# Kernel tuning notes

Measured on AMD Instinct MI355X. Metric: run time of the kernel, lower is better.

## Reference

```python
import jax
import jax.numpy as jnp
from jax import lax
import numpy as np

N_LAYER = 8
SCALE = 4
H_CH = 128
Z_CH = 64


def conv2d(x, w, b=None, stride=1, pad=0):
    # x: NCHW, w: OIHW
    out = lax.conv_general_dilated(
        x, w, (stride, stride), [(pad, pad), (pad, pad)],
        dimension_numbers=("NCHW", "OIHW", "NCHW"))
    if b is not None:
        out = out + b[None, :, None, None]
    return out


def conv_transpose2d(x, w, stride):
    # torch ConvTranspose2d semantics, weight shape (in, out, kH, kW), no bias
    return lax.conv_transpose(
        x, w, (stride, stride), "VALID",
        dimension_numbers=("NCHW", "IOHW", "NCHW"), transpose_kernel=True)


def lstm_cell(inp, hidden, cell, gw, gb, tw, tb):
    # inp = inp + transform(hidden); gates fused into one conv (order f,i,o,s)
    inp = inp + conv2d(hidden, tw, tb, pad=2)
    gates = conv2d(inp, gw, gb, pad=2)
    f, i, o, s = jnp.split(gates, 4, axis=1)
    cell = jax.nn.sigmoid(f) * cell + jax.nn.sigmoid(i) * jnp.tanh(s)
    hidden = jax.nn.sigmoid(o) * jnp.tanh(cell)
    return hidden, cell


def setup_inputs() -> dict:
    key = jax.random.key(0)
    ks = jax.random.split(key, 24)
    b, xc, H, W = 64, 3, 64, 64
    vd, rd = 7, 256
    hs, ws = H // SCALE, W // SCALE
    enc_in = vd + rd + xc + H_CH   # 394
    dec_in = vd + rd + Z_CH        # 327

    def w_init(k, shape):
        fan_in = int(np.prod(shape[1:]))
        return jax.random.normal(k, shape, jnp.float32) / np.sqrt(fan_in)

    inp = {
        "x": jax.random.normal(ks[0], (b, xc, H, W), jnp.float32),
        "v": jax.random.normal(ks[1], (b, vd), jnp.float32),
        "r": jax.random.normal(ks[2], (b, rd, hs, ws), jnp.float32),
        "eps": jax.random.normal(ks[3], (N_LAYER, b, Z_CH, hs, ws), jnp.float32),
        "read_w": w_init(ks[4], (xc, xc, SCALE, SCALE)),
        "write_w": w_init(ks[5], (H_CH, H_CH, SCALE, SCALE)),  # (in,out,kH,kW)
        "prior_w": w_init(ks[6], (2 * Z_CH, H_CH, 5, 5)),
        "prior_b": jnp.zeros((2 * Z_CH,), jnp.float32),
        "post_w": w_init(ks[7], (2 * Z_CH, H_CH, 5, 5)),
        "post_b": jnp.zeros((2 * Z_CH,), jnp.float32),
        "enc_gw": w_init(ks[8], (4 * H_CH, enc_in, 5, 5)),
        "enc_gb": jnp.zeros((4 * H_CH,), jnp.float32),
        "enc_tw": w_init(ks[9], (enc_in, H_CH, 5, 5)),
        "enc_tb": jnp.zeros((enc_in,), jnp.float32),
        "dec_gw": w_init(ks[10], (4 * H_CH, dec_in, 5, 5)),
        "dec_gb": jnp.zeros((4 * H_CH,), jnp.float32),
        "dec_tw": w_init(ks[11], (dec_in, H_CH, 5, 5)),
        "dec_tb": jnp.zeros((dec_in,), jnp.float32),
        "obs_w": w_init(ks[12], (xc, H_CH, 1, 1)),
        "obs_b": jnp.zeros((xc,), jnp.float32),
    }
    return inp


def reference(x, v, r, eps, read_w, write_w, prior_w, prior_b, post_w, post_b,
              enc_gw, enc_gb, enc_tw, enc_tb, dec_gw, dec_gb, dec_tw, dec_tb,
              obs_w, obs_b):
    b, _, H, W = x.shape
    hs, ws = H // SCALE, W // SCALE
    dt = x.dtype
    h_enc = jnp.zeros((b, H_CH, hs, ws), dt)
    c_enc = jnp.zeros((b, H_CH, hs, ws), dt)
    h_dec = jnp.zeros((b, H_CH, hs, ws), dt)
    c_dec = jnp.zeros((b, H_CH, hs, ws), dt)
    u = jnp.zeros((b, H_CH, H, W), dt)

    xr = conv2d(x, read_w, stride=SCALE)            # (b, xc, hs, ws)
    vb = jnp.broadcast_to(v[:, :, None, None], (b, v.shape[1], hs, ws))
    rb = r if r.shape[2] == hs else jnp.tile(r, (1, 1, hs, ws))

    kl_loss = jnp.zeros((), dt)
    for t in range(N_LAYER):
        p_mu, p_lv = jnp.split(conv2d(h_dec, prior_w, prior_b, pad=2), 2, axis=1)
        h_enc, c_enc = lstm_cell(
            jnp.concatenate([h_dec, xr, vb, rb], axis=1),
            h_enc, c_enc, enc_gw, enc_gb, enc_tw, enc_tb)
        q_mu, q_lv = jnp.split(conv2d(h_enc, post_w, post_b, pad=2), 2, axis=1)
        z = q_mu + jnp.exp(0.5 * q_lv) * eps[t]
        h_dec, c_dec = lstm_cell(
            jnp.concatenate([z, vb, rb], axis=1),
            h_dec, c_dec, dec_gw, dec_gb, dec_tw, dec_tb)
        u = u + conv_transpose2d(h_dec, write_w, SCALE)
        # KL(q||p) with var = exp(logvar); log(var1/var0) = p_lv - q_lv
        kl = 0.5 * (jnp.exp(q_lv - p_lv)
                    + (p_mu - q_mu) ** 2 * jnp.exp(-p_lv)
                    - 1.0 + (p_lv - q_lv))
        kl_loss = kl_loss + kl.sum(axis=(1, 2, 3)).mean()

    canvas = jax.nn.sigmoid(conv2d(u, obs_w, obs_b))
    return canvas, kl_loss
```

## Files before the change

### kernel.cpp

```cpp
#include <hip/hip_runtime.h>
#include <hip/hip_bf16.h>

using bf16 = __hip_bfloat16;
typedef __attribute__((ext_vector_type(8))) short short8;
typedef __attribute__((ext_vector_type(4))) float f32x4;
typedef __attribute__((ext_vector_type(8))) int i32x8;
typedef __attribute__((ext_vector_type(4))) int i32x4;

#define DEVI __device__ __forceinline__

#define MTOT 16384
#define PADS 25600

DEVI float sigm_(float x){ return 1.f/(1.f+expf(-x)); }

DEVI long pidx_(int m){
  int nb = m>>8, iy=(m>>4)&15, ix=m&15;
  return (long)(nb*20 + iy + 2)*20 + (ix + 2);
}

DEVI unsigned char f2fp8(float x){
  int p = __builtin_amdgcn_cvt_pk_fp8_f32(x, 0.f, 0, false);
  return (unsigned char)(p & 0xFF);
}
DEVI float fp82f(unsigned char v){
  return __builtin_amdgcn_cvt_f32_fp8((int)v, 0);
}

DEVI void async16(const void* g, void* l) {
  __builtin_amdgcn_global_load_lds(
      (__attribute__((address_space(1))) void*)(unsigned long long)g,
      (__attribute__((address_space(3))) void*)(unsigned int)(unsigned long long)l,
      16, 0, 0);
}

template<int N> DEVI void waitbar(){
  if constexpr (N==0)      asm volatile("s_waitcnt vmcnt(0)\ns_barrier" ::: "memory");
  else if constexpr (N==3) asm volatile("s_waitcnt vmcnt(3)\ns_barrier" ::: "memory");
  else                     asm volatile("s_waitcnt vmcnt(6)\ns_barrier" ::: "memory");
}

template<int CA, int NS>
DEVI void g8_core(const unsigned char* __restrict__ A8,
                  const unsigned char* __restrict__ Bt8,
                  int m0, int n0, unsigned char* AsB, unsigned char* BsB,
                  f32x4 (&acc)[4][4])
{
  constexpr int Kp8 = NS*128;
  const int tid = threadIdx.x;
  const int wv = tid>>6, ln = tid&63;

  const int rr = tid>>3;
  const int lc = (tid&7) ^ (rr&7);
  long paRC[4], pbR[4];
  #pragma unroll
  for (int i=0;i<4;i++){
    int m = m0 + rr + (i<<5);
    paRC[i] = (long)(((m>>8)*20 + ((m>>4)&15))*20 + (m&15)) * CA;
    pbR[i]  = (long)(n0 + rr + (i<<5))*Kp8 + lc*16;
  }

  int cc = lc*16, tp = 0, ks = 0;
  auto stage = [&](int d){
    const int shiftC = ((tp/5)*20 + (tp%5)) * CA;
    char* la = (char*)AsB + d*16384 + (wv<<10);
    char* lb = (char*)BsB + d*16384 + (wv<<10);
    #pragma unroll
    for (int i=0;i<4;i++) async16(A8 + paRC[i] + shiftC + cc, la + i*4096);
    #pragma unroll
    for (int i=0;i<4;i++) async16(Bt8 + pbR[i] + ks, lb + i*4096);
    cc += 128; if (cc >= CA){ cc -= CA; tp++; }
    ks += 128;
  };

  const int wm = wv>>1, wn = wv&1;
  const int rA0 = (wm<<6) + (ln&15);
  const int rB0 = (wn<<6) + (ln&15);
  const int xa = ln&7;
  const int q2 = (ln>>4)<<1;
  const int c0 = ((q2    ) ^ xa)<<4;
  const int c1 = ((q2 | 1) ^ xa)<<4;

  stage(0);
  for (int t=0; t<NS; ++t) {
    asm volatile("s_waitcnt vmcnt(0)\ns_barrier" ::: "memory");
    if (t+1 < NS) stage((t+1)&1);

    const char* as_ = (const char*)AsB + (t&1)*16384;
    const char* bs_ = (const char*)BsB + (t&1)*16384;
    i32x8 af[4], bfr[4];
    #pragma unroll
    for (int f=0; f<4; f++){
      const char* p = as_ + ((rA0 + (f<<4))<<7);
      ((i32x4*)&af[f])[0] = *(const i32x4*)(p + c0);
      ((i32x4*)&af[f])[1] = *(const i32x4*)(p + c1);
    }
    #pragma unroll
    for (int f=0; f<4; f++){
      const char* p = bs_ + ((rB0 + (f<<4))<<7);
      ((i32x4*)&bfr[f])[0] = *(const i32x4*)(p + c0);
      ((i32x4*)&bfr[f])[1] = *(const i32x4*)(p + c1);
    }
    __builtin_amdgcn_s_setprio(1);
    #pragma unroll
    for (int mf=0; mf<4; mf++)
      #pragma unroll
      for (int nf=0; nf<4; nf++)
        acc[mf][nf] = __builtin_amdgcn_mfma_scale_f32_16x16x128_f8f6f4(
            af[mf], bfr[nf], acc[mf][nf], 0, 0, 0, 127, 0, 122);
    __builtin_amdgcn_s_setprio(0);
  }
}

template<int CA, int NS>
__global__ __launch_bounds__(256)
void conv_g8(const unsigned char* __restrict__ A8,
             const unsigned char* __restrict__ Bt8,
             const float* __restrict__ bias, bf16* __restrict__ outB)
{
  __shared__ alignas(16) unsigned char As[2][16384];
  __shared__ alignas(16) unsigned char Bs[2][16384];
  const int m0 = blockIdx.x<<7, n0 = blockIdx.y<<7;
  f32x4 acc[4][4] = {};
  g8_core<CA,NS>(A8, Bt8, m0, n0, &As[0][0], &Bs[0][0], acc);

  const int tid = threadIdx.x;
  const int wv = tid>>6, ln = tid&63;
  const int mb = m0 + ((wv>>1)<<6);
  const int nb = n0 + ((wv&1)<<6);
  const int ml = (ln>>4)<<2;
  const int nl = ln&15;
  #pragma unroll
  for (int mf=0; mf<4; mf++)
    #pragma unroll
    for (int j=0; j<4; j++) {
      const int m = mb + (mf<<4) + ml + j;
      #pragma unroll
      for (int nf=0; nf<4; nf++) {
        const int n = nb + (nf<<4) + nl;
        outB[((long)m<<9) + n] = __float2bfloat16(acc[mf][nf][j] + bias[n]);
      }
    }
}

__global__ __launch_bounds__(256)
void conv_tp8(const unsigned char* __restrict__ h8Dec,
              const unsigned char* __restrict__ h8Enc,
              const unsigned char* __restrict__ Bt8DP,
              const unsigned char* __restrict__ Bt8EncT,
              const float* __restrict__ dec_tb, const float* __restrict__ prior_b,
              const float* __restrict__ enc_tb,
              float* __restrict__ PriorO,
              unsigned char* __restrict__ sDec8, const bf16* __restrict__ STdec,
              unsigned char* __restrict__ sEnc8, const bf16* __restrict__ STenc,
              const bf16* __restrict__ hDecB,
              const float* __restrict__ Wc, float* __restrict__ uc)
{
  __shared__ alignas(16) unsigned char As[2][16384];
  __shared__ alignas(16) unsigned char Bs[2][16384];
  const int z = blockIdx.z;
  const int m0 = blockIdx.x<<7, n0 = blockIdx.y<<7;
  f32x4 acc[4][4] = {};
  if (z == 0) g8_core<128,25>(h8Dec, Bt8DP,   m0, n0, &As[0][0], &Bs[0][0], acc);
  else        g8_core<128,25>(h8Enc, Bt8EncT, m0, n0, &As[0][0], &Bs[0][0], acc);

  const int tid = threadIdx.x;
  const int wv = tid>>6, ln = tid&63;
  const int mb = m0 + ((wv>>1)<<6);
  const int nb = n0 + ((wv&1)<<6);
  const int ml = (ln>>4)<<2;
  const int nl = ln&15;
  #pragma unroll
  for (int mf=0; mf<4; mf++)
    #pragma unroll
    for (int j=0; j<4; j++) {
      const int m = mb + (mf<<4) + ml + j;
      const long pI = pidx_(m);
      #pragma unroll
      for (int nf=0; nf<4; nf++) {
        const int n = nb + (nf<<4) + nl;
        const float v = acc[mf][nf][j];
        if (z == 0) {
          if (n < 352) {
            float b  = (n < 327) ? dec_tb[n] : 0.f;
            float st = __bfloat162float(STdec[(long)m*352 + n]);
            sDec8[pI*352 + n] = f2fp8(v + b + st);
          } else if (n >= 384) {
            PriorO[((long)m<<7) + (n-384)] = v + prior_b[n-384];
          }
        } else {
          if (n < 416) {
            float b  = (n < 394) ? enc_tb[n] : 0.f;
            float st = __bfloat162float(STenc[(long)m*416 + n]);
            float e  = (n < 128) ? __bfloat162float(hDecB[(pI<<7) + n]) : 0.f;
            sEnc8[pI*416 + n] = f2fp8(v + b + st + e);
          }
        }
      }
    }

  const int gid = blockIdx.z*512 + blockIdx.y*128 + blockIdx.x;
  const int m = (gid<<4) + (tid>>4);
  const int pix = tid&15;
  const int nb2 = m>>8, iy=(m>>4)&15, ix=m&15;
  const bf16* __restrict__ h = hDecB + (pidx_(m)<<7);
  float a0=0.f, a1=0.f, a2=0.f;
  #pragma unroll 4
  for (int c=0;c<128;c++) {
    float hv = __bfloat162float(h[c]);
    const float* wl = Wc + c*48 + pix*3;
    a0 += hv*wl[0]; a1 += hv*wl[1]; a2 += hv*wl[2];
  }
  const int ki = pix>>2, kj = pix&3;
  long ob = ((long)((nb2<<6) + (iy<<2) + ki)*64 + (ix<<2) + kj)*3;
  uc[ob+0] += a0; uc[ob+1] += a1; uc[ob+2] += a2;
}

template<int CA, int EPI>
DEVI void conv_body(const bf16* __restrict__ A, const bf16* __restrict__ Bt,
                    bf16* __restrict__ outB,
                    int s0, int s1, int m0, int n0,
                    bf16* AsBase, bf16* BsBase)
{
  constexpr int Kp = 25*CA;
  const int NS = s1 - s0;

  const int tid = threadIdx.x;
  const int wv = tid>>6, ln = tid&63;

  const int rA = tid>>2;
  const int qs = ((tid&3) ^ ((rA>>1)&3))<<3;
  const int mA0 = m0 + rA, mA1 = m0 + 128 + rA;
  const long paA0 = ((long)(((mA0>>8)*20 + ((mA0>>4)&15))*20 + (mA0&15)))*CA + qs;
  const long paA1 = ((long)(((mA1>>8)*20 + ((mA1>>4)&15))*20 + (mA1&15)))*CA + qs;
  const long pbB  = (long)(n0 + rA)*Kp + qs;

  int kk0 = s0*32;
  int c0 = kk0 % CA;
  int tap = kk0 / CA;
  int kh = tap/5, kw = tap%5;
  int ks = kk0;

  auto stage = [&](int d){
    const long sh = (long)(kh*20 + kw)*CA + c0;
    char* la = (char*)AsBase + d*16384 + (wv<<10);
    char* lb = (char*)BsBase + d*8192  + (wv<<10);
    async16(A + paA0 + sh, la);
    async16(A + paA1 + sh, la + 8192);
    async16(Bt + pbB + ks, lb);
    ks += 32;
    c0 += 32; if (c0==CA){ c0=0; if(++kw==5){kw=0; ++kh;} }
  };

  f32x4 acc[4][4] = {};
  const int wm = wv>>1, wn = wv&1;
  const int rowA = (wm<<6) + (ln&15);
  const int rowB = (wn<<6) + (ln&15);
  const int kqA = (((ln>>4) ^ ((rowA>>1)&3))<<4);
  const int kqB = (((ln>>4) ^ ((rowB>>1)&3))<<4);

  stage(0); stage(1);
  int bc = 0, bs = 2;
  for (int t=0; t<NS; ++t) {
    if (t+1 < NS) waitbar<3>();
    else          waitbar<0>();
    if (t+2 < NS) stage(bs);

    const char* as_ = (const char*)AsBase + bc*16384;
    const char* bs_ = (const char*)BsBase + bc*8192;
    short8 af[4], bfr[4];
    #pragma unroll
    for (int mf=0; mf<4; mf++)
      af[mf] = *(const short8*)(as_ + ((rowA + (mf<<4))<<6) + kqA);
    #pragma unroll
    for (int nf=0; nf<4; nf++)
      bfr[nf] = *(const short8*)(bs_ + ((rowB + (nf<<4))<<6) + kqB);
    __builtin_amdgcn_s_setprio(1);
    #pragma unroll
    for (int mf=0; mf<4; mf++)
      #pragma unroll
      for (int nf=0; nf<4; nf++)
        acc[mf][nf] = __builtin_amdgcn_mfma_f32_16x16x32_bf16(af[mf], bfr[nf], acc[mf][nf], 0,0,0);
    __builtin_amdgcn_s_setprio(0);
    bc = (bc==2)?0:bc+1; bs = (bs==2)?0:bs+1;
  }

  const int mb = m0 + (wm<<6);
  const int nb = n0 + (wn<<6);
  const int ml = (ln>>4)<<2;
  const int nl = ln&15;
  #pragma unroll
  for (int mf=0; mf<4; mf++)
    #pragma unroll
    for (int j=0; j<4; j++) {
      const int m = mb + (mf<<4) + ml + j;
      #pragma unroll
      for (int nf=0; nf<4; nf++) {
        const int n = nb + (nf<<4) + nl;
        outB[((long)m<<7) + n] = __float2bfloat16(acc[mf][nf][j]);
      }
    }
}

__global__ __launch_bounds__(512)
void conv_post(const bf16* __restrict__ hEnc, const bf16* __restrict__ BtPost,
               bf16* __restrict__ PP)
{
  __shared__ alignas(16) bf16 As[3][256*32];
  __shared__ alignas(16) bf16 Bs[3][128*32];
  const int z = blockIdx.z;
  conv_body<128,6>(hEnc, BtPost, PP + (long)z*MTOT*128,
                   z*25, z*25+25, blockIdx.x<<8, 0, &As[0][0], &Bs[0][0]);
}

__global__ void repack_w_k(const float* __restrict__ w, bf16* __restrict__ Bt,
                           int O, int I, int CA, long total)
{
  long e = (long)blockIdx.x*256 + threadIdx.x;
  if (e >= total) return;
  const int Kp = 25*CA;
  int o = (int)(e / Kp);
  int k = (int)(e % Kp);
  int blk = k / CA, c = k % CA;
  float v = 0.f;
  if (o < O && c < I) v = w[((long)o*I + c)*25 + blk];
  Bt[e] = __float2bfloat16(v);
}

__global__ void repack_w8_k(const float* __restrict__ w, unsigned char* __restrict__ Bt,
                            int O, int I, int CA, int Kp8, long total)
{
  long e = (long)blockIdx.x*256 + threadIdx.x;
  if (e >= total) return;
  int o = (int)(e / Kp8);
  int k = (int)(e % Kp8);
  float v = 0.f;
  if (k < 25*CA) {
    int blk = k / CA, c = k % CA;
    if (o < O && c < I) v = w[((long)o*I + c)*25 + blk] * 32.0f;
  }
  Bt[e] = f2fp8(v);
}

__global__ void wcomb_k(const float* __restrict__ ww, const float* __restrict__ ow,
                        float* __restrict__ Wc)
{
  int idx = blockIdx.x*256 + threadIdx.x;
  if (idx >= 128*48) return;
  int c = idx / 48, rst = idx % 48;
  int pix = rst / 3, o = rst % 3;
  int ki = pix >> 2, kj = pix & 3;
  float a = 0.f;
  for (int mm=0; mm<128; mm++)
    a += ww[(((long)c*128 + mm)*4 + ki)*4 + kj] * ow[o*128 + mm];
  Wc[idx] = a;
}

__global__ void xr_k(const float* __restrict__ x, const float* __restrict__ rw,
                     float* __restrict__ xr)
{
  int idx = blockIdx.x*256 + threadIdx.x;
  if (idx >= MTOT*3) return;
  int m = idx / 3, o = idx % 3;
  int nb = m>>8, iy=(m>>4)&15, ix=m&15;
  float a = 0.f;
  for (int c=0;c<3;c++)
    for (int kh=0;kh<4;kh++)
      for (int kw=0;kw<4;kw++)
        a += x[((long)(nb*3+c)*64 + (iy*4+kh))*64 + (ix*4+kw)] * rw[((o*3+c)*4+kh)*4+kw];
  xr[idx] = a;
}

__global__ void st_enc_k(const float* __restrict__ xr, const float* __restrict__ v,
                         const float* __restrict__ r, bf16* __restrict__ ST)
{
  long g = (long)blockIdx.x*256 + threadIdx.x;
  if (g >= (long)MTOT*266) return;
  int m = (int)(g / 266), ch = (int)(g % 266);
  int nb = m>>8, sp = m&255;
  float val;
  if (ch < 3)       val = xr[m*3 + ch];
  else if (ch < 10) val = v[nb*7 + ch - 3];
  else              val = r[((long)nb*256 + (ch-10))*256 + sp];
  ST[(long)m*416 + 128 + ch] = __float2bfloat16(val);
}

__global__ void st_dec_k(const float* __restrict__ v, const float* __restrict__ r,
                         bf16* __restrict__ ST)
{
  long g = (long)blockIdx.x*256 + threadIdx.x;
  if (g >= (long)MTOT*263) return;
  int m = (int)(g / 263), ch = (int)(g % 263);
  int nb = m>>8, sp = m&255;
  float val;
  if (ch < 7) val = v[nb*7 + ch];
  else        val = r[((long)nb*256 + (ch-7))*256 + sp];
  ST[(long)m*352 + 64 + ch] = __float2bfloat16(val);
}

__global__ void lstm_k(const bf16* __restrict__ gates, float* __restrict__ cbuf,
                       bf16* __restrict__ hpad, unsigned char* __restrict__ h8)
{
  int idx = blockIdx.x*256 + threadIdx.x;
  int m = idx >> 7, c = idx & 127;
  long gb = (long)m << 9;
  float f = __bfloat162float(gates[gb + c]);
  float i = __bfloat162float(gates[gb + 128 + c]);
  float o = __bfloat162float(gates[gb + 256 + c]);
  float s = __bfloat162float(gates[gb + 384 + c]);
  float cell = sigm_(f)*cbuf[idx] + sigm_(i)*tanhf(s);
  cbuf[idx] = cell;
  float h = sigm_(o)*tanhf(cell);
  long hp = (pidx_(m)<<7) + c;
  hpad[hp] = __float2bfloat16(h);
  h8[hp] = f2fp8(h);
}

__global__ void zkl4_k(const bf16* __restrict__ PP, const float* __restrict__ pb,
                       const float* __restrict__ prior, const float* __restrict__ eps_t,
                       unsigned char* __restrict__ sDec8, float* __restrict__ part)
{
  __shared__ float wsum[4];
  const long PL = (long)MTOT*128;
  int idx = blockIdx.x*256 + threadIdx.x;
  int m = idx >> 6, c = idx & 63;
  float qm = pb[c], ql = pb[64 + c];
  #pragma unroll
  for (int z=0; z<4; ++z) {
    qm += __bfloat162float(PP[z*PL + ((long)m<<7) + c]);
    ql += __bfloat162float(PP[z*PL + ((long)m<<7) + 64 + c]);
  }
  long pbx = (long)m << 7;
  float pm = prior[pbx + c], pl = prior[pbx + 64 + c];
  int nb = m>>8, sp = m&255;
  float e = eps_t[((long)nb*64 + c)*256 + sp];
  float z = qm + expf(0.5f*ql)*e;
  long so = pidx_(m)*352 + c;
  sDec8[so] = f2fp8(fp82f(sDec8[so]) + z);
  float kl = expf(ql - pl) + (pm-qm)*(pm-qm)*expf(-pl) - 1.f + (pl - ql);
  #pragma unroll
  for (int off=32; off>0; off>>=1) kl += __shfl_down(kl, off);
  if ((threadIdx.x & 63) == 0) wsum[threadIdx.x >> 6] = kl;
  __syncthreads();
  if (threadIdx.x == 0)
    part[blockIdx.x] = wsum[0] + wsum[1] + wsum[2] + wsum[3];
}

__global__ __launch_bounds__(256)
void wrc_k(const bf16* __restrict__ hpad, const float* __restrict__ Wc,
           float* __restrict__ uc)
{
  __shared__ float Wl[128*48];
  for (int i = threadIdx.x; i < 128*48; i += 256) Wl[i] = Wc[i];
  __syncthreads();
  int t = threadIdx.x;
  int mloc = t >> 4, pix = t & 15;
  int m = (blockIdx.x<<4) + mloc;
  int nb = m>>8, iy=(m>>4)&15, ix=m&15;
  const bf16* h = hpad + (pidx_(m)<<7);
  float a0=0.f, a1=0.f, a2=0.f;
  for (int c=0;c<128;c++) {
    float hv = __bfloat162float(h[c]);
    const float* wl = Wl + c*48 + pix*3;
    a0 += hv*wl[0]; a1 += hv*wl[1]; a2 += hv*wl[2];
  }
  int ki = pix>>2, kj = pix&3;
  long ob = ((long)((nb<<6) + (iy<<2) + ki)*64 + (ix<<2) + kj)*3;
  uc[ob+0] += a0; uc[ob+1] += a1; uc[ob+2] += a2;
}

__global__ void canvas_k(const float* __restrict__ uc, const float* __restrict__ ob,
                         float* __restrict__ out)
{
  int idx = blockIdx.x*256 + threadIdx.x;
  int x = idx & 63, y = (idx>>6)&63;
  int rem = idx >> 12;
  int o = rem % 3, n = rem / 3;
  float v = uc[((long)((n<<6)+y)*64 + x)*3 + o] + ob[o];
  out[idx] = 1.f/(1.f+expf(-v));
}

__global__ void klred_k(const float* __restrict__ part, float* __restrict__ out)
{
  __shared__ float wsum[4];
  float a = 0.f;
  for (int i = threadIdx.x; i < 32768; i += 256) a += part[i];
  #pragma unroll
  for (int off=32; off>0; off>>=1) a += __shfl_down(a, off);
  if ((threadIdx.x & 63) == 0) wsum[threadIdx.x >> 6] = a;
  __syncthreads();
  if (threadIdx.x == 0)
    out[786432] = (wsum[0] + wsum[1] + wsum[2] + wsum[3]) * (0.5f/64.f);
}

static const long O_BT_POST  = 0;
static const long O_BT_ENCT  = O_BT_POST  + 819200;
static const long O_BT_DP    = O_BT_ENCT  + 3276800;
static const long O_BT_ENCG  = O_BT_DP    + 3276800;
static const long O_BT_DECG  = O_BT_ENCG  + 10649600;
static const long O_WCOMB    = O_BT_DECG  + 9011200;
static const long O_XR       = O_WCOMB    + 24576;
static const long O_KLP      = O_XR       + 196608;
static const long O_STENC    = O_KLP      + 131072;
static const long O_STDEC    = O_STENC    + 13631488;
static const long O_HENC     = O_STDEC    + 11534336;
static const long O_HDEC     = O_HENC     + 6553600;
static const long O_SENC     = O_HDEC     + 6553600;
static const long O_SDEC     = O_SENC     + 21299200;
static const long O_CENC     = O_SDEC     + 18022400;
static const long O_CDEC     = O_CENC     + 8388608;
static const long O_PRIOR    = O_CDEC     + 8388608;
static const long O_H8E      = O_PRIOR    + 8388608;
static const long O_H8D      = O_H8E      + 3276800;
static const long O_PG       = O_H8D      + 3276800;
static const long O_UC       = O_PG       + 33554432;
static const long WS_TOTAL   = O_UC       + 3145728;

extern "C" void kernel_launch(void* const* d_in, const int* in_sizes, int n_in,
                              void* d_out, int out_size, void* d_ws, size_t ws_size,
                              hipStream_t stream)
{
  const float* x       = (const float*)d_in[0];
  const float* v       = (const float*)d_in[1];
  const float* r       = (const float*)d_in[2];
  const float* eps     = (const float*)d_in[3];
  const float* read_w  = (const float*)d_in[4];
  const float* write_w = (const float*)d_in[5];
  const float* prior_w = (const float*)d_in[6];
  const float* prior_b = (const float*)d_in[7];
  const float* post_w  = (const float*)d_in[8];
  const float* post_b  = (const float*)d_in[9];
  const float* enc_gw  = (const float*)d_in[10];
  const float* enc_gb  = (const float*)d_in[11];
  const float* enc_tw  = (const float*)d_in[12];
  const float* enc_tb  = (const float*)d_in[13];
  const float* dec_gw  = (const float*)d_in[14];
  const float* dec_gb  = (const float*)d_in[15];
  const float* dec_tw  = (const float*)d_in[16];
  const float* dec_tb  = (const float*)d_in[17];
  const float* obs_w   = (const float*)d_in[18];
  const float* obs_b   = (const float*)d_in[19];

  char* ws = (char*)d_ws;
  bf16* BtPost  = (bf16*)(ws + O_BT_POST);
  unsigned char* Bt8EncT = (unsigned char*)(ws + O_BT_ENCT);
  unsigned char* Bt8DP   = (unsigned char*)(ws + O_BT_DP);
  unsigned char* Bt8EncG = (unsigned char*)(ws + O_BT_ENCG);
  unsigned char* Bt8DecG = (unsigned char*)(ws + O_BT_DECG);
  float* Wcomb  = (float*)(ws + O_WCOMB);
  float* XR     = (float*)(ws + O_XR);
  float* KLpart = (float*)(ws + O_KLP);
  bf16* STenc   = (bf16*)(ws + O_STENC);
  bf16* STdec   = (bf16*)(ws + O_STDEC);
  bf16* hEnc    = (bf16*)(ws + O_HENC);
  bf16* hDec    = (bf16*)(ws + O_HDEC);
  unsigned char* sEnc8 = (unsigned char*)(ws + O_SENC);
  unsigned char* sDec8 = (unsigned char*)(ws + O_SDEC);
  float* cEnc   = (float*)(ws + O_CENC);
  float* cDec   = (float*)(ws + O_CDEC);
  float* PriorO = (float*)(ws + O_PRIOR);
  unsigned char* h8Enc = (unsigned char*)(ws + O_H8E);
  unsigned char* h8Dec = (unsigned char*)(ws + O_H8D);
  bf16* Gates   = (bf16*)(ws + O_PG);
  bf16* PostP   = (bf16*)(ws + O_PG + 16777216);
  float* Ucomb  = (float*)(ws + O_UC);
  float* out    = (float*)d_out;

  size_t clr = (size_t)WS_TOTAL; if (clr > ws_size) clr = ws_size;
  hipMemsetAsync(d_ws, 0, clr, stream);

  repack_w_k<<<1600, 256, 0, stream>>>(post_w, BtPost, 128, 128, 128, 128L*3200);
  repack_w8_k<<<6400, 256, 0, stream>>>(enc_tw, Bt8EncT, 394, 128, 128, 3200, 512L*3200);
  repack_w8_k<<<4800, 256, 0, stream>>>(dec_tw, Bt8DP, 327, 128, 128, 3200, 384L*3200);
  repack_w8_k<<<1600, 256, 0, stream>>>(prior_w, Bt8DP + 384L*3200, 128, 128, 128, 3200, 128L*3200);
  repack_w8_k<<<20992, 256, 0, stream>>>(enc_gw, Bt8EncG, 512, 394, 416, 82*128, 512L*10496);
  repack_w8_k<<<17664, 256, 0, stream>>>(dec_gw, Bt8DecG, 512, 327, 352, 69*128, 512L*8832);
  wcomb_k<<<24, 256, 0, stream>>>(write_w, obs_w, Wcomb);
  xr_k<<<192, 256, 0, stream>>>(x, read_w, XR);
  st_enc_k<<<(int)(((long)MTOT*266 + 255)/256), 256, 0, stream>>>(XR, v, r, STenc);
  st_dec_k<<<(int)(((long)MTOT*263 + 255)/256), 256, 0, stream>>>(v, r, STdec);

  for (int t = 0; t < 8; ++t) {
    conv_tp8<<<dim3(128,4,2), 256, 0, stream>>>(
        h8Dec, h8Enc, Bt8DP, Bt8EncT, dec_tb, prior_b, enc_tb,
        PriorO, sDec8, STdec, sEnc8, STenc, hDec, Wcomb, Ucomb);
    conv_g8<416,82><<<dim3(128,4), 256, 0, stream>>>(sEnc8, Bt8EncG, enc_gb, Gates);
    lstm_k<<<8192, 256, 0, stream>>>(Gates, cEnc, hEnc, h8Enc);
    conv_post<<<dim3(64,1,4), 512, 0, stream>>>(hEnc, BtPost, PostP);
    zkl4_k<<<4096, 256, 0, stream>>>(PostP, post_b, PriorO,
                                     eps + (long)t*64*64*256, sDec8,
                                     KLpart + (long)t*4096);
    conv_g8<352,69><<<dim3(128,4), 256, 0, stream>>>(sDec8, Bt8DecG, dec_gb, Gates);
    lstm_k<<<8192, 256, 0, stream>>>(Gates, cDec, hDec, h8Dec);
  }

  wrc_k<<<1024, 256, 0, stream>>>(hDec, Wcomb, Ucomb);
  canvas_k<<<3072, 256, 0, stream>>>(Ucomb, obs_b, out);
  klred_k<<<1, 256, 0, stream>>>(KLpart, out);
}
```

Baseline: 2.685 ms.

## Vectorize LSTM kernel and fuse write-conv accumulation into decoder LSTM

The LSTM pointwise kernel now handles 8 channels per thread, using 16-byte gate loads, vector cell-state loads and stores, and packed fp8 writes. The per-step canvas write convolution, which used to sit at the tail of conv_tp8 and read hDec from global memory, moves into a new lstm_wrc_k kernel. That kernel stages the fresh decoder hidden state and the combined weights in shared memory and accumulates into Ucomb right after the decoder LSTM. This removes the extra work from the GEMM kernel's epilogue and the separate final wrc_k launch. In exchange, each LSTM block now loads the 24KB weight table into LDS on every step.

New measurement: 2.620 ms. 2.5% less time.

```diff
diff --git a/kernel.cpp b/kernel.cpp
--- a/kernel.cpp
+++ b/kernel.cpp
@@ -6,6 +6,7 @@
 typedef __attribute__((ext_vector_type(4))) float f32x4;
 typedef __attribute__((ext_vector_type(8))) int i32x8;
 typedef __attribute__((ext_vector_type(4))) int i32x4;
+typedef __attribute__((ext_vector_type(2))) int i32x2;
 
 #define DEVI __device__ __forceinline__
 
@@ -13,6 +14,11 @@
 #define PADS 25600
 
 DEVI float sigm_(float x){ return 1.f/(1.f+expf(-x)); }
+
+DEVI float s2f(short v){
+  unsigned u = ((unsigned)(unsigned short)v) << 16;
+  return __builtin_bit_cast(float, u);
+}
 
 DEVI long pidx_(int m){
   int nb = m>>8, iy=(m>>4)&15, ix=m&15;
@@ -153,8 +159,7 @@
               float* __restrict__ PriorO,
               unsigned char* __restrict__ sDec8, const bf16* __restrict__ STdec,
               unsigned char* __restrict__ sEnc8, const bf16* __restrict__ STenc,
-              const bf16* __restrict__ hDecB,
-              const float* __restrict__ Wc, float* __restrict__ uc)
+              const bf16* __restrict__ hDecB)
 {
   __shared__ alignas(16) unsigned char As[2][16384];
   __shared__ alignas(16) unsigned char Bs[2][16384];
@@ -198,22 +203,6 @@
         }
       }
     }
-
-  const int gid = blockIdx.z*512 + blockIdx.y*128 + blockIdx.x;
-  const int m = (gid<<4) + (tid>>4);
-  const int pix = tid&15;
-  const int nb2 = m>>8, iy=(m>>4)&15, ix=m&15;
-  const bf16* __restrict__ h = hDecB + (pidx_(m)<<7);
-  float a0=0.f, a1=0.f, a2=0.f;
-  #pragma unroll 4
-  for (int c=0;c<128;c++) {
-    float hv = __bfloat162float(h[c]);
-    const float* wl = Wc + c*48 + pix*3;
-    a0 += hv*wl[0]; a1 += hv*wl[1]; a2 += hv*wl[2];
-  }
-  const int ki = pix>>2, kj = pix&3;
-  long ob = ((long)((nb2<<6) + (iy<<2) + ki)*64 + (ix<<2) + kj)*3;
-  uc[ob+0] += a0; uc[ob+1] += a1; uc[ob+2] += a2;
 }
 
 template<int CA, int EPI>
@@ -398,22 +387,86 @@
   ST[(long)m*352 + 64 + ch] = __float2bfloat16(val);
 }
 
-__global__ void lstm_k(const bf16* __restrict__ gates, float* __restrict__ cbuf,
-                       bf16* __restrict__ hpad, unsigned char* __restrict__ h8)
-{
-  int idx = blockIdx.x*256 + threadIdx.x;
-  int m = idx >> 7, c = idx & 127;
-  long gb = (long)m << 9;
-  float f = __bfloat162float(gates[gb + c]);
-  float i = __bfloat162float(gates[gb + 128 + c]);
-  float o = __bfloat162float(gates[gb + 256 + c]);
-  float s = __bfloat162float(gates[gb + 384 + c]);
-  float cell = sigm_(f)*cbuf[idx] + sigm_(i)*tanhf(s);
-  cbuf[idx] = cell;
-  float h = sigm_(o)*tanhf(cell);
-  long hp = (pidx_(m)<<7) + c;
-  hpad[hp] = __float2bfloat16(h);
-  h8[hp] = f2fp8(h);
+DEVI void lstm8_(const bf16* __restrict__ gates, float* __restrict__ cbuf,
+                 bf16* __restrict__ hpad, unsigned char* __restrict__ h8,
+                 int m, int c0, float* hout)
+{
+  long gb = ((long)m<<9) + c0;
+  short8 gf = *(const short8*)(gates + gb);
+  short8 gi = *(const short8*)(gates + gb + 128);
+  short8 go = *(const short8*)(gates + gb + 256);
+  short8 gs = *(const short8*)(gates + gb + 384);
+  float* cb = cbuf + ((long)m<<7) + c0;
+  f32x4 cv0 = *(f32x4*)cb;
+  f32x4 cv1 = *(f32x4*)(cb+4);
+  short8 hh;
+  #pragma unroll
+  for (int j=0;j<8;j++){
+    float f = s2f(gf[j]);
+    float i = s2f(gi[j]);
+    float o = s2f(go[j]);
+    float s = s2f(gs[j]);
+    float cell = sigm_(f)*((j<4)?cv0[j]:cv1[j-4]) + sigm_(i)*tanhf(s);
+    if (j<4) cv0[j]=cell; else cv1[j-4]=cell;
+    float h = sigm_(o)*tanhf(cell);
+    hout[j] = h;
+    bf16 hb = __float2bfloat16(h);
+    hh[j] = __builtin_bit_cast(short, hb);
+  }
+  *(f32x4*)cb = cv0;
+  *(f32x4*)(cb+4) = cv1;
+  long hp = (pidx_(m)<<7) + c0;
+  *(short8*)(hpad + hp) = hh;
+  int w0 = __builtin_amdgcn_cvt_pk_fp8_f32(hout[0], hout[1], 0, false);
+  w0 = __builtin_amdgcn_cvt_pk_fp8_f32(hout[2], hout[3], w0, true);
+  int w1 = __builtin_amdgcn_cvt_pk_fp8_f32(hout[4], hout[5], 0, false);
+  w1 = __builtin_amdgcn_cvt_pk_fp8_f32(hout[6], hout[7], w1, true);
+  i32x2 pw; pw[0]=w0; pw[1]=w1;
+  *(i32x2*)(h8 + hp) = pw;
+}
+
+__global__ __launch_bounds__(256)
+void lstm_k(const bf16* __restrict__ gates, float* __restrict__ cbuf,
+            bf16* __restrict__ hpad, unsigned char* __restrict__ h8)
+{
+  const int tid = threadIdx.x;
+  const int m = (blockIdx.x<<4) + (tid>>4);
+  const int c0 = (tid&15)<<3;
+  float h[8];
+  lstm8_(gates, cbuf, hpad, h8, m, c0, h);
+}
+
+__global__ __launch_bounds__(256)
+void lstm_wrc_k(const bf16* __restrict__ gates, float* __restrict__ cbuf,
+                bf16* __restrict__ hpad, unsigned char* __restrict__ h8,
+                const float* __restrict__ Wc, float* __restrict__ uc)
+{
+  __shared__ float Wl[6144];
+  __shared__ float hl[16*128];
+  const int tid = threadIdx.x;
+  for (int i = tid; i < 6144; i += 256) Wl[i] = Wc[i];
+  const int mloc = tid>>4;
+  const int m = (blockIdx.x<<4) + mloc;
+  const int c0 = (tid&15)<<3;
+  float h[8];
+  lstm8_(gates, cbuf, hpad, h8, m, c0, h);
+  #pragma unroll
+  for (int j=0;j<8;j++) hl[(mloc<<7) + c0 + j] = h[j];
+  __syncthreads();
+
+  const int pix = tid&15;
+  const float* hrow = hl + (mloc<<7);
+  float a0=0.f, a1=0.f, a2=0.f;
+  #pragma unroll 4
+  for (int c=0;c<128;c++) {
+    float hv = hrow[c];
+    const float* wl = Wl + c*48 + pix*3;
+    a0 += hv*wl[0]; a1 += hv*wl[1]; a2 += hv*wl[2];
+  }
+  const int nb = m>>8, iy=(m>>4)&15, ix=m&15;
+  const int ki = pix>>2, kj = pix&3;
+  long ob = ((long)((nb<<6) + (iy<<2) + ki)*64 + (ix<<2) + kj)*3;
+  uc[ob+0] += a0; uc[ob+1] += a1; uc[ob+2] += a2;
 }
 
 __global__ void zkl4_k(const bf16* __restrict__ PP, const float* __restrict__ pb,
@@ -444,29 +497,6 @@
   __syncthreads();
   if (threadIdx.x == 0)
     part[blockIdx.x] = wsum[0] + wsum[1] + wsum[2] + wsum[3];
-}
-
-__global__ __launch_bounds__(256)
-void wrc_k(const bf16* __restrict__ hpad, const float* __restrict__ Wc,
-           float* __restrict__ uc)
-{
-  __shared__ float Wl[128*48];
-  for (int i = threadIdx.x; i < 128*48; i += 256) Wl[i] = Wc[i];
-  __syncthreads();
-  int t = threadIdx.x;
-  int mloc = t >> 4, pix = t & 15;
-  int m = (blockIdx.x<<4) + mloc;
-  int nb = m>>8, iy=(m>>4)&15, ix=m&15;
-  const bf16* h = hpad + (pidx_(m)<<7);
-  float a0=0.f, a1=0.f, a2=0.f;
-  for (int c=0;c<128;c++) {
-    float hv = __bfloat162float(h[c]);
-    const float* wl = Wl + c*48 + pix*3;
-    a0 += hv*wl[0]; a1 += hv*wl[1]; a2 += hv*wl[2];
-  }
-  int ki = pix>>2, kj = pix&3;
-  long ob = ((long)((nb<<6) + (iy<<2) + ki)*64 + (ix<<2) + kj)*3;
-  uc[ob+0] += a0; uc[ob+1] += a1; uc[ob+2] += a2;
 }
 
 __global__ void canvas_k(const float* __restrict__ uc, const float* __restrict__ ob,
@@ -583,18 +613,17 @@
   for (int t = 0; t < 8; ++t) {
     conv_tp8<<<dim3(128,4,2), 256, 0, stream>>>(
         h8Dec, h8Enc, Bt8DP, Bt8EncT, dec_tb, prior_b, enc_tb,
-        PriorO, sDec8, STdec, sEnc8, STenc, hDec, Wcomb, Ucomb);
+        PriorO, sDec8, STdec, sEnc8, STenc, hDec);
     conv_g8<416,82><<<dim3(128,4), 256, 0, stream>>>(sEnc8, Bt8EncG, enc_gb, Gates);
-    lstm_k<<<8192, 256, 0, stream>>>(Gates, cEnc, hEnc, h8Enc);
+    lstm_k<<<1024, 256, 0, stream>>>(Gates, cEnc, hEnc, h8Enc);
     conv_post<<<dim3(64,1,4), 512, 0, stream>>>(hEnc, BtPost, PostP);
     zkl4_k<<<4096, 256, 0, stream>>>(PostP, post_b, PriorO,
                                      eps + (long)t*64*64*256, sDec8,
                                      KLpart + (long)t*4096);
     conv_g8<352,69><<<dim3(128,4), 256, 0, stream>>>(sDec8, Bt8DecG, dec_gb, Gates);
-    lstm_k<<<8192, 256, 0, stream>>>(Gates, cDec, hDec, h8Dec);
-  }
-
-  wrc_k<<<1024, 256, 0, stream>>>(hDec, Wcomb, Ucomb);
+    lstm_wrc_k<<<1024, 256, 0, stream>>>(Gates, cDec, hDec, h8Dec, Wcomb, Ucomb);
+  }
+
   canvas_k<<<3072, 256, 0, stream>>>(Ucomb, obs_b, out);
   klred_k<<<1, 256, 0, stream>>>(KLpart, out);
 }
```
